# Optimization experiments

Measured on AMD Instinct MI355X. Metric: run time of the kernel, lower is better.

Reference implementation:

```python
import jax, jax.numpy as jnp
import numpy as np
import math

B, S, HID = 2, 1024, 2048
N_HEAD, N_KV = 16, 4
HEAD = HID // N_HEAD          # 128
N_REP = N_HEAD // N_KV        # 4


def setup_inputs() -> dict:
    key = jax.random.key(0)
    ks = jax.random.split(key, 5)
    x = jax.random.normal(ks[0], (B, S, HID), dtype=jnp.float32)
    # realistic RoPE tables: freqs over half dim, duplicated (rotate_half convention)
    inv_freq = 1.0 / (10000.0 ** (np.arange(0, HEAD, 2, dtype=np.float32) / HEAD))
    t = np.arange(S, dtype=np.float32)
    freqs = np.outer(t, inv_freq)                    # [S, HEAD/2]
    emb = np.concatenate([freqs, freqs], axis=-1)    # [S, HEAD]
    cos = jnp.asarray(np.cos(emb), dtype=jnp.float32)
    sin = jnp.asarray(np.sin(emb), dtype=jnp.float32)
    sc = 0.02
    wq = jax.random.normal(ks[1], (HID, HID), dtype=jnp.float32) * sc
    wk = jax.random.normal(ks[2], (HID, N_KV * HEAD), dtype=jnp.float32) * sc
    wv = jax.random.normal(ks[3], (HID, N_KV * HEAD), dtype=jnp.float32) * sc
    wo = jax.random.normal(ks[4], (HID, HID), dtype=jnp.float32) * sc
    return {"x": x, "cos": cos, "sin": sin, "wq": wq, "wk": wk, "wv": wv, "wo": wo}


def _rotate_half(t):
    h = t.shape[-1] // 2
    return jnp.concatenate([-t[..., h:], t[..., :h]], axis=-1)


def reference(x, cos, sin, wq, wk, wv, wo):
    b, s, _ = x.shape
    q = (x @ wq).reshape(b, s, N_HEAD, HEAD)   # [B,S,H,D]
    k = (x @ wk).reshape(b, s, N_KV, HEAD)     # [B,S,Kv,D]
    v = (x @ wv).reshape(b, s, N_KV, HEAD)
    # RoPE: cos/sin [S,D] -> [S,1,D], broadcasts over batch and heads
    c = cos[:s, None, :]
    sn = sin[:s, None, :]
    q = q * c + _rotate_half(q) * sn
    k = k * c + _rotate_half(k) * sn
    # GQA: repeat kv heads to match query heads
    k = jnp.repeat(k, N_REP, axis=2)           # [B,S,H,D]
    v = jnp.repeat(v, N_REP, axis=2)
    q = q.transpose(0, 2, 1, 3)                # [B,H,S,D]
    k = k.transpose(0, 2, 1, 3)
    v = v.transpose(0, 2, 1, 3)
    scores = jnp.einsum("bhqd,bhkd->bhqk", q, k) / math.sqrt(HEAD)
    causal = jnp.triu(jnp.full((s, s), -jnp.inf, dtype=scores.dtype), k=1)
    scores = scores + causal[None, None, :, :]
    probs = jax.nn.softmax(scores.astype(jnp.float32), axis=-1).astype(q.dtype)
    out = jnp.einsum("bhqk,bhkd->bhqd", probs, v)   # [B,H,S,D]
    out = out.transpose(0, 2, 1, 3).reshape(b, s, N_HEAD * HEAD)
    return out @ wo
```

## Files before the change

### kernel.cpp

```cpp
#include <hip/hip_runtime.h>
#include <hip/hip_bf16.h>
#include <math.h>
#include <stdint.h>

#define BATCH 2
#define SEQ   1024
#define HID   2048
#define NH    16
#define NKV   4
#define HEAD  128
#define MROWS (BATCH*SEQ)
#define QSC   0.08838834764831845f

typedef _Float16 f16;
typedef _Float16 f16x8 __attribute__((ext_vector_type(8)));
typedef __fp16   h16x2 __attribute__((ext_vector_type(2)));
typedef float    f32x4 __attribute__((ext_vector_type(4)));

__device__ __forceinline__ void glds16(const void* g, void* l) {
    __builtin_amdgcn_global_load_lds(
        (const __attribute__((address_space(1))) void*)g,
        (__attribute__((address_space(3))) void*)l, 16, 0, 0);
}

__device__ __forceinline__ f32x4 mfma16(f16x8 a, f16x8 b, f32x4 c) {
    return __builtin_amdgcn_mfma_f32_16x16x32_f16(a, b, c, 0, 0, 0);
}

__global__ __launch_bounds__(256)
void prep(const float* __restrict__ x,
          const float* __restrict__ wq, const float* __restrict__ wk,
          const float* __restrict__ wv, const float* __restrict__ wo,
          f16* __restrict__ x16, f16* __restrict__ Wqkvt, f16* __restrict__ Wot)
{
    __shared__ float t[64][65];
    const int bid = blockIdx.x, tid = threadIdx.x;
    if (bid < 4096) {
        int i = bid * 256 + tid;
        float4 v = ((const float4*)x)[i];
        union { ushort4 u; f16 h[4]; } o;
        o.h[0] = (f16)v.x; o.h[1] = (f16)v.y; o.h[2] = (f16)v.z; o.h[3] = (f16)v.w;
        ((ushort4*)x16)[i] = o.u;
        return;
    }
    const float* W; int ld, cs, k0, n0; f16* out;
    if (bid < 5632) {
        int b2 = bid - 4096;
        n0 = (b2 % 48) * 64; k0 = (b2 / 48) * 64; out = Wqkvt;
        if (n0 < 2048)      { W = wq; ld = 2048; cs = n0; }
        else if (n0 < 2560) { W = wk; ld = 512;  cs = n0 - 2048; }
        else                { W = wv; ld = 512;  cs = n0 - 2560; }
    } else {
        int b3 = bid - 5632;
        n0 = (b3 % 32) * 64; k0 = (b3 / 32) * 64; out = Wot;
        W = wo; ld = 2048; cs = n0;
    }
    const int tr = tid >> 4, tc = tid & 15;
    #pragma unroll
    for (int i = 0; i < 4; ++i) {
        int row = tr * 4 + i;
        float4 v = *(const float4*)&W[(size_t)(k0 + row) * ld + cs + tc * 4];
        t[row][tc*4+0] = v.x; t[row][tc*4+1] = v.y;
        t[row][tc*4+2] = v.z; t[row][tc*4+3] = v.w;
    }
    __syncthreads();
    #pragma unroll
    for (int i = 0; i < 4; ++i) {
        int nrow = tr * 4 + i;
        union { ushort4 u; f16 h[4]; } o;
        o.h[0] = (f16)t[tc*4+0][nrow]; o.h[1] = (f16)t[tc*4+1][nrow];
        o.h[2] = (f16)t[tc*4+2][nrow]; o.h[3] = (f16)t[tc*4+3][nrow];
        *(ushort4*)&out[(size_t)(n0 + nrow) * 2048 + k0 + tc * 4] = o.u;
    }
}

template<int MODE>
__global__ __launch_bounds__(256)
void gemm16(const f16* __restrict__ A, const f16* __restrict__ Bt,
            f16* __restrict__ Oq, f16* __restrict__ Ok, f16* __restrict__ Ov,
            float* __restrict__ Of, int ntn)
{
    __shared__ f16 As[2][128 * 64];
    __shared__ f16 Bs[2][64 * 64];
    const int tid   = threadIdx.x;
    const int lane  = tid & 63;
    const int wid   = tid >> 6;
    const int col_l = lane & 15;
    const int hi    = lane >> 4;

    const int nwg = gridDim.x;
    const int cpx = nwg >> 3;
    const int bid = blockIdx.x;
    const int sw  = (bid & 7) * cpx + (bid >> 3);
    const int n0  = (sw % ntn) * 64;
    const int m0  = (sw / ntn) * 128;

    f32x4 acc[2][4];
    #pragma unroll
    for (int mt = 0; mt < 2; ++mt)
        #pragma unroll
        for (int nt = 0; nt < 4; ++nt)
            acc[mt][nt] = (f32x4){0.f, 0.f, 0.f, 0.f};

    auto stage = [&](int buf, int kt) {
        #pragma unroll
        for (int j = 0; j < 4; ++j) {
            int gidx = j * 256 + tid;
            int r = gidx >> 3, g = gidx & 7;
            int gs = (g ^ (r & 7)) << 3;
            glds16(A + (size_t)(m0 + r) * 2048 + kt * 64 + gs,
                   (char*)&As[buf][0] + (size_t)(j * 256 + (wid << 6)) * 16);
        }
        #pragma unroll
        for (int j = 0; j < 2; ++j) {
            int gidx = j * 256 + tid;
            int r = gidx >> 3, g = gidx & 7;
            int gs = (g ^ (r & 7)) << 3;
            glds16(Bt + (size_t)(n0 + r) * 2048 + kt * 64 + gs,
                   (char*)&Bs[buf][0] + (size_t)(j * 256 + (wid << 6)) * 16);
        }
    };

    stage(0, 0);
    stage(1, 1);

    const int ar0 = wid * 32 + col_l;
    const int ar1 = ar0 + 16;

    int cur = 0;
    #pragma unroll 1
    for (int kt = 0; kt < 32; ++kt) {
        if (kt < 31) asm volatile("s_waitcnt vmcnt(6)" ::: "memory");
        else         asm volatile("s_waitcnt vmcnt(0)" ::: "memory");
        __builtin_amdgcn_s_barrier();
        __builtin_amdgcn_sched_barrier(0);

        #pragma unroll
        for (int ks = 0; ks < 2; ++ks) {
            int gr = (ks << 2) | hi;
            f16x8 a0 = *(const f16x8*)&As[cur][ar0 * 64 + ((gr ^ (ar0 & 7)) << 3)];
            f16x8 a1 = *(const f16x8*)&As[cur][ar1 * 64 + ((gr ^ (ar1 & 7)) << 3)];
            #pragma unroll
            for (int nt = 0; nt < 4; ++nt) {
                int br = nt * 16 + col_l;
                f16x8 b = *(const f16x8*)&Bs[cur][br * 64 + ((gr ^ (br & 7)) << 3)];
                acc[0][nt] = mfma16(a0, b, acc[0][nt]);
                acc[1][nt] = mfma16(a1, b, acc[1][nt]);
            }
        }

        asm volatile("s_waitcnt lgkmcnt(0)" ::: "memory");
        __builtin_amdgcn_sched_barrier(0);
        __builtin_amdgcn_s_barrier();
        if (kt + 2 < 32) stage(cur, kt + 2);
        cur ^= 1;
    }

    if (MODE == 0) {
        #pragma unroll
        for (int mt = 0; mt < 2; ++mt)
            #pragma unroll
            for (int r = 0; r < 4; ++r) {
                int grow = m0 + wid * 32 + mt * 16 + hi * 4 + r;
                #pragma unroll
                for (int nt = 0; nt < 4; ++nt)
                    Of[(size_t)grow * 2048 + n0 + nt * 16 + col_l] = acc[mt][nt][r];
            }
    } else if (n0 < 2048) {
        #pragma unroll
        for (int mt = 0; mt < 2; ++mt)
            #pragma unroll
            for (int r = 0; r < 4; ++r) {
                int grow = m0 + wid * 32 + mt * 16 + hi * 4 + r;
                #pragma unroll
                for (int nt = 0; nt < 4; ++nt)
                    Oq[(size_t)grow * 2048 + n0 + nt * 16 + col_l] = (f16)acc[mt][nt][r];
            }
    } else if (n0 < 2560) {
        #pragma unroll
        for (int mt = 0; mt < 2; ++mt)
            #pragma unroll
            for (int r = 0; r < 4; ++r) {
                int grow = m0 + wid * 32 + mt * 16 + hi * 4 + r;
                #pragma unroll
                for (int nt = 0; nt < 4; ++nt)
                    Ok[(size_t)grow * 512 + (n0 - 2048) + nt * 16 + col_l] = (f16)acc[mt][nt][r];
            }
    } else {
        #pragma unroll
        for (int mt = 0; mt < 2; ++mt) {
            int grow0 = m0 + wid * 32 + mt * 16 + hi * 4;
            int bb = grow0 >> 10, s0 = grow0 & (SEQ - 1);
            #pragma unroll
            for (int nt = 0; nt < 4; ++nt) {
                int vcol = (n0 - 2560) + nt * 16 + col_l;
                int kvh = vcol >> 7, d = vcol & 127;
                union { ushort4 u; f16 h[4]; } pv;
                #pragma unroll
                for (int r = 0; r < 4; ++r) pv.h[r] = (f16)acc[mt][nt][r];
                *(ushort4*)&Ov[(size_t)((bb * 4 + kvh) * 128 + d) * 1024 + s0] = pv.u;
            }
        }
    }
}

__global__ __launch_bounds__(256)
void rope_k(f16* __restrict__ k16,
            const float* __restrict__ cosp, const float* __restrict__ sinp)
{
    int t = blockIdx.x * 256 + threadIdx.x;
    int row = t >> 6; int rem = t & 63; int head = rem >> 4; int quad = rem & 15;
    f16* p = k16 + (size_t)row * 512 + head * 128 + quad * 4;
    const int srow = row & (SEQ - 1);
    const int d0 = quad * 4;
    float4 c4 = *(const float4*)&cosp[srow * HEAD + d0];
    float4 s4 = *(const float4*)&sinp[srow * HEAD + d0];
    union { ushort4 u; f16 h[4]; } lo, hv, olo, ohi;
    lo.u = *(ushort4*)p;
    hv.u = *(ushort4*)(p + 64);
    const float c[4] = {c4.x, c4.y, c4.z, c4.w};
    const float s[4] = {s4.x, s4.y, s4.z, s4.w};
    #pragma unroll
    for (int e = 0; e < 4; ++e) {
        float fl = (float)lo.h[e], fh = (float)hv.h[e];
        olo.h[e] = (f16)(fl * c[e] - fh * s[e]);
        ohi.h[e] = (f16)(fh * c[e] + fl * s[e]);
    }
    *(ushort4*)p        = olo.u;
    *(ushort4*)(p + 64) = ohi.u;
}

__global__ __launch_bounds__(256, 2)
void attn16(const f16* __restrict__ q16, const f16* __restrict__ k16,
            const f16* __restrict__ vT,
            const float* __restrict__ cosp, const float* __restrict__ sinp,
            f16* __restrict__ attnb)
{
    __shared__ f16 Ks[2][64 * 128];
    __shared__ f16 Vs[2][128 * 64];

    const int tid   = threadIdx.x;
    const int lane  = tid & 63;
    const int wid   = tid >> 6;
    const int col_l = lane & 15;
    const int hi    = lane >> 4;

    const int bx = blockIdx.x;
    const int r8 = bx >> 8;
    const int c  = bx & 255;
    const int bh = c >> 3;
    const int j8 = c & 7;
    const int qt = r8 ? j8 : (15 - j8);
    const int b  = bh >> 4;
    const int h  = bh & 15;
    const int kv = h >> 2;
    const int qrow = qt * 64 + wid * 16 + col_l;

    f16x8 qf[4];
    {
        const f16* qp = q16 + (size_t)(b * SEQ + qrow) * 2048 + h * 128 + hi * 8;
        f16x8 raw[4];
        #pragma unroll
        for (int ks = 0; ks < 4; ++ks) raw[ks] = *(const f16x8*)&qp[ks * 32];
        #pragma unroll
        for (int ks = 0; ks < 2; ++ks) {
            union { float4 v; float a[4]; } c0, c1, s0, s1;
            const float* cp = cosp + qrow * HEAD + ks * 32 + hi * 8;
            const float* sp = sinp + qrow * HEAD + ks * 32 + hi * 8;
            c0.v = *(const float4*)cp;  c1.v = *(const float4*)(cp + 4);
            s0.v = *(const float4*)sp;  s1.v = *(const float4*)(sp + 4);
            #pragma unroll
            for (int e = 0; e < 8; ++e) {
                float cc = (e < 4) ? c0.a[e & 3] : c1.a[e & 3];
                float sv = (e < 4) ? s0.a[e & 3] : s1.a[e & 3];
                float lo = (float)raw[ks][e], hv = (float)raw[ks + 2][e];
                qf[ks][e]     = (f16)((lo * cc - hv * sv) * QSC);
                qf[ks + 2][e] = (f16)((hv * cc + lo * sv) * QSC);
            }
        }
    }
    const f16* vTg = vT + (size_t)(b * 4 + kv) * 128 * 1024;

    auto stage = [&](int buf, int kt) {
        #pragma unroll
        for (int j = 0; j < 4; ++j) {
            int gidx = j * 256 + tid;
            int r = gidx >> 4, g = gidx & 15;
            glds16(k16 + (size_t)(b * SEQ + kt * 64 + r) * 512 + kv * 128 + ((g ^ (r & 7)) << 3),
                   (char*)&Ks[buf][0] + (size_t)(j * 256 + (wid << 6)) * 16);
        }
        #pragma unroll
        for (int j = 0; j < 4; ++j) {
            int gidx = j * 256 + tid;
            int d = gidx >> 3, g = gidx & 7;
            glds16(vTg + (size_t)d * 1024 + kt * 64 + ((g ^ (d & 7)) << 3),
                   (char*)&Vs[buf][0] + (size_t)(j * 256 + (wid << 6)) * 16);
        }
    };

    f32x4 O[8];
    #pragma unroll
    for (int dt = 0; dt < 8; ++dt) O[dt] = (f32x4){0.f, 0.f, 0.f, 0.f};
    float mrun = -INFINITY, lrun = 0.f;

    const int ntiles = qt + 1;
    stage(0, 0);
    asm volatile("s_waitcnt vmcnt(0)" ::: "memory");
    __syncthreads();

    int cur = 0;
    #pragma unroll 1
    for (int kt = 0; kt < ntiles; ++kt) {
        if (kt + 1 < ntiles) stage(cur ^ 1, kt + 1);

        f32x4 S[4];
        #pragma unroll
        for (int t = 0; t < 4; ++t) S[t] = (f32x4){0.f, 0.f, 0.f, 0.f};
        #pragma unroll
        for (int ks = 0; ks < 4; ++ks) {
            int gr = (ks << 2) | hi;
            #pragma unroll
            for (int t = 0; t < 4; ++t) {
                int rr = t * 16 + col_l;
                f16x8 kf = *(const f16x8*)&Ks[cur][rr * 128 + ((gr ^ (rr & 7)) << 3)];
                S[t] = mfma16(kf, qf[ks], S[t]);
            }
        }
        float p[16];
        #pragma unroll
        for (int t = 0; t < 4; ++t) {
            p[t*4+0] = S[t][0]; p[t*4+1] = S[t][1];
            p[t*4+2] = S[t][2]; p[t*4+3] = S[t][3];
        }

        if (kt == qt) {
            #pragma unroll
            for (int sl = 0; sl < 16; ++sl) {
                int kk = kt * 64 + (sl >> 2) * 16 + hi * 4 + (sl & 3);
                if (kk > qrow) p[sl] = -INFINITY;
            }
        }

        float mt = p[0];
        #pragma unroll
        for (int sl = 1; sl < 16; ++sl) mt = fmaxf(mt, p[sl]);
        mt = fmaxf(mt, __shfl_xor(mt, 16));
        mt = fmaxf(mt, __shfl_xor(mt, 32));
        float mnew = fmaxf(mrun, mt);
        float corr = __expf(mrun - mnew);
        mrun = mnew;
        float ps = 0.f;
        #pragma unroll
        for (int sl = 0; sl < 16; ++sl) { p[sl] = __expf(p[sl] - mnew); ps += p[sl]; }
        ps += __shfl_xor(ps, 16);
        ps += __shfl_xor(ps, 32);
        lrun = lrun * corr + ps;

        union U2 { h16x2 h; int i; };
        int pk[8];
        #pragma unroll
        for (int t = 0; t < 4; ++t) {
            { U2 u; u.h = __builtin_amdgcn_cvt_pkrtz(p[t*4+0], p[t*4+1]); pk[t*2+0] = u.i; }
            { U2 u; u.h = __builtin_amdgcn_cvt_pkrtz(p[t*4+2], p[t*4+3]); pk[t*2+1] = u.i; }
        }
        union UA { f16x8 v; int i[4]; } F0, F1;
        #pragma unroll
        for (int j = 0; j < 4; ++j) {
            int srcl = col_l + 16 * ((2 * hi + (j >> 1)) & 3);
            int a0 = __builtin_amdgcn_ds_bpermute(srcl << 2, pk[j & 1]);
            int a1 = __builtin_amdgcn_ds_bpermute(srcl << 2, pk[2 + (j & 1)]);
            F0.i[j] = (hi >= 2) ? a1 : a0;
            int b0 = __builtin_amdgcn_ds_bpermute(srcl << 2, pk[4 + (j & 1)]);
            int b1 = __builtin_amdgcn_ds_bpermute(srcl << 2, pk[6 + (j & 1)]);
            F1.i[j] = (hi >= 2) ? b1 : b0;
        }

        float cb[4];
        #pragma unroll
        for (int r = 0; r < 4; ++r)
            cb[r] = __int_as_float(__builtin_amdgcn_ds_bpermute((hi * 4 + r) << 2,
                                                                __float_as_int(corr)));
        #pragma unroll
        for (int dt = 0; dt < 8; ++dt) {
            O[dt][0] *= cb[0]; O[dt][1] *= cb[1];
            O[dt][2] *= cb[2]; O[dt][3] *= cb[3];
        }

        #pragma unroll
        for (int dt = 0; dt < 8; ++dt) {
            int vr = dt * 16 + col_l;
            f16x8 v0 = *(const f16x8*)&Vs[cur][vr * 64 + ((hi ^ (vr & 7)) << 3)];
            O[dt] = mfma16(F0.v, v0, O[dt]);
            f16x8 v1 = *(const f16x8*)&Vs[cur][vr * 64 + (((4 | hi) ^ (vr & 7)) << 3)];
            O[dt] = mfma16(F1.v, v1, O[dt]);
        }

        if (kt + 1 < ntiles) {
            asm volatile("s_waitcnt vmcnt(0)" ::: "memory");
            __syncthreads();
            cur ^= 1;
        }
    }

    float linv = 1.f / lrun;
    float lb[4];
    #pragma unroll
    for (int r = 0; r < 4; ++r)
        lb[r] = __int_as_float(__builtin_amdgcn_ds_bpermute((hi * 4 + r) << 2,
                                                            __float_as_int(linv)));
    #pragma unroll
    for (int dt = 0; dt < 8; ++dt)
        #pragma unroll
        for (int r = 0; r < 4; ++r) {
            int row = b * SEQ + qt * 64 + wid * 16 + hi * 4 + r;
            attnb[(size_t)row * 2048 + h * 128 + dt * 16 + col_l] = (f16)(O[dt][r] * lb[r]);
        }
}

extern "C" void kernel_launch(void* const* d_in, const int* in_sizes, int n_in,
                              void* d_out, int out_size, void* d_ws, size_t ws_size,
                              hipStream_t stream)
{
    const float* x    = (const float*)d_in[0];
    const float* cosp = (const float*)d_in[1];
    const float* sinp = (const float*)d_in[2];
    const float* wq   = (const float*)d_in[3];
    const float* wk   = (const float*)d_in[4];
    const float* wv   = (const float*)d_in[5];
    const float* wo   = (const float*)d_in[6];
    float* out = (float*)d_out;

    char* ws = (char*)d_ws;
    f16* x16    = (f16*)(ws);
    f16* attn16v= (f16*)(ws);
    f16* Wqkvt  = (f16*)(ws + 8388608);
    f16* q16    = (f16*)(ws + 20971520);
    f16* k16    = (f16*)(ws + 29360128);
    f16* vT     = (f16*)(ws + 31457280);
    f16* Wot    = (f16*)(ws + 33554432);

    prep<<<6656, 256, 0, stream>>>(x, wq, wk, wv, wo, x16, Wqkvt, Wot);

    gemm16<1><<<768, 256, 0, stream>>>(x16, Wqkvt, q16, k16, vT, nullptr, 48);

    rope_k<<<512, 256, 0, stream>>>(k16, cosp, sinp);

    attn16<<<512, 256, 0, stream>>>(q16, k16, vT, cosp, sinp, attn16v);

    gemm16<0><<<512, 256, 0, stream>>>(attn16v, Wot, nullptr, nullptr, nullptr, out, 32);
}
```

Measured before the change: 203.7 us.

## Give each attention wave two 16-row query groups with lazy softmax rescaling

The attention kernel drops to two waves of 128 threads per block, and each wave now handles 32 query rows as two 16-row groups. Each K and V fragment read from LDS feeds two MFMAs, so LDS traffic per FLOP is roughly halved. It also skips the output rescale when the running max has risen by no more than 8 (a threshold in the lazy style), and raises wave priority around the MFMA sections. The cost is higher register pressure, fewer waves per block for latency hiding, and the staging work falls on fewer threads.

```diff
diff --git a/kernel.cpp b/kernel.cpp
--- a/kernel.cpp
+++ b/kernel.cpp
@@ -230,7 +230,7 @@
     *(ushort4*)(p + 64) = ohi.u;
 }
 
-__global__ __launch_bounds__(256, 2)
+__global__ __launch_bounds__(128)
 void attn16(const f16* __restrict__ q16, const f16* __restrict__ k16,
             const f16* __restrict__ vT,
             const float* __restrict__ cosp, const float* __restrict__ sinp,
@@ -254,10 +254,12 @@
     const int b  = bh >> 4;
     const int h  = bh & 15;
     const int kv = h >> 2;
-    const int qrow = qt * 64 + wid * 16 + col_l;
-
-    f16x8 qf[4];
-    {
+    const int qbase = qt * 64 + wid * 32;
+
+    f16x8 qf[2][4];
+    #pragma unroll
+    for (int g = 0; g < 2; ++g) {
+        const int qrow = qbase + g * 16 + col_l;
         const f16* qp = q16 + (size_t)(b * SEQ + qrow) * 2048 + h * 128 + hi * 8;
         f16x8 raw[4];
         #pragma unroll
@@ -274,8 +276,8 @@
                 float cc = (e < 4) ? c0.a[e & 3] : c1.a[e & 3];
                 float sv = (e < 4) ? s0.a[e & 3] : s1.a[e & 3];
                 float lo = (float)raw[ks][e], hv = (float)raw[ks + 2][e];
-                qf[ks][e]     = (f16)((lo * cc - hv * sv) * QSC);
-                qf[ks + 2][e] = (f16)((hv * cc + lo * sv) * QSC);
+                qf[g][ks][e]     = (f16)((lo * cc - hv * sv) * QSC);
+                qf[g][ks + 2][e] = (f16)((hv * cc + lo * sv) * QSC);
             }
         }
     }
@@ -283,25 +285,27 @@
 
     auto stage = [&](int buf, int kt) {
         #pragma unroll
-        for (int j = 0; j < 4; ++j) {
-            int gidx = j * 256 + tid;
+        for (int j = 0; j < 8; ++j) {
+            int gidx = j * 128 + tid;
             int r = gidx >> 4, g = gidx & 15;
             glds16(k16 + (size_t)(b * SEQ + kt * 64 + r) * 512 + kv * 128 + ((g ^ (r & 7)) << 3),
-                   (char*)&Ks[buf][0] + (size_t)(j * 256 + (wid << 6)) * 16);
-        }
-        #pragma unroll
-        for (int j = 0; j < 4; ++j) {
-            int gidx = j * 256 + tid;
+                   (char*)&Ks[buf][0] + (size_t)(j * 128 + (wid << 6)) * 16);
+        }
+        #pragma unroll
+        for (int j = 0; j < 8; ++j) {
+            int gidx = j * 128 + tid;
             int d = gidx >> 3, g = gidx & 7;
             glds16(vTg + (size_t)d * 1024 + kt * 64 + ((g ^ (d & 7)) << 3),
-                   (char*)&Vs[buf][0] + (size_t)(j * 256 + (wid << 6)) * 16);
+                   (char*)&Vs[buf][0] + (size_t)(j * 128 + (wid << 6)) * 16);
         }
     };
 
-    f32x4 O[8];
-    #pragma unroll
-    for (int dt = 0; dt < 8; ++dt) O[dt] = (f32x4){0.f, 0.f, 0.f, 0.f};
-    float mrun = -INFINITY, lrun = 0.f;
+    f32x4 O[2][8];
+    #pragma unroll
+    for (int g = 0; g < 2; ++g)
+        #pragma unroll
+        for (int dt = 0; dt < 8; ++dt) O[g][dt] = (f32x4){0.f, 0.f, 0.f, 0.f};
+    float m0 = -INFINITY, m1 = -INFINITY, l0 = 0.f, l1 = 0.f;
 
     const int ntiles = qt + 1;
     stage(0, 0);
@@ -313,9 +317,13 @@
     for (int kt = 0; kt < ntiles; ++kt) {
         if (kt + 1 < ntiles) stage(cur ^ 1, kt + 1);
 
-        f32x4 S[4];
-        #pragma unroll
-        for (int t = 0; t < 4; ++t) S[t] = (f32x4){0.f, 0.f, 0.f, 0.f};
+        f32x4 S0[4], S1[4];
+        #pragma unroll
+        for (int t = 0; t < 4; ++t) {
+            S0[t] = (f32x4){0.f, 0.f, 0.f, 0.f};
+            S1[t] = (f32x4){0.f, 0.f, 0.f, 0.f};
+        }
+        __builtin_amdgcn_s_setprio(1);
         #pragma unroll
         for (int ks = 0; ks < 4; ++ks) {
             int gr = (ks << 2) | hi;
@@ -323,77 +331,108 @@
             for (int t = 0; t < 4; ++t) {
                 int rr = t * 16 + col_l;
                 f16x8 kf = *(const f16x8*)&Ks[cur][rr * 128 + ((gr ^ (rr & 7)) << 3)];
-                S[t] = mfma16(kf, qf[ks], S[t]);
-            }
-        }
-        float p[16];
-        #pragma unroll
-        for (int t = 0; t < 4; ++t) {
-            p[t*4+0] = S[t][0]; p[t*4+1] = S[t][1];
-            p[t*4+2] = S[t][2]; p[t*4+3] = S[t][3];
-        }
+                S0[t] = mfma16(kf, qf[0][ks], S0[t]);
+                S1[t] = mfma16(kf, qf[1][ks], S1[t]);
+            }
+        }
+        __builtin_amdgcn_s_setprio(0);
+
+        float p0[16], p1[16];
+        #pragma unroll
+        for (int t = 0; t < 4; ++t)
+            #pragma unroll
+            for (int r = 0; r < 4; ++r) {
+                p0[t*4+r] = S0[t][r];
+                p1[t*4+r] = S1[t][r];
+            }
 
         if (kt == qt) {
             #pragma unroll
             for (int sl = 0; sl < 16; ++sl) {
                 int kk = kt * 64 + (sl >> 2) * 16 + hi * 4 + (sl & 3);
-                if (kk > qrow) p[sl] = -INFINITY;
-            }
-        }
-
-        float mt = p[0];
-        #pragma unroll
-        for (int sl = 1; sl < 16; ++sl) mt = fmaxf(mt, p[sl]);
-        mt = fmaxf(mt, __shfl_xor(mt, 16));
-        mt = fmaxf(mt, __shfl_xor(mt, 32));
-        float mnew = fmaxf(mrun, mt);
-        float corr = __expf(mrun - mnew);
-        mrun = mnew;
-        float ps = 0.f;
-        #pragma unroll
-        for (int sl = 0; sl < 16; ++sl) { p[sl] = __expf(p[sl] - mnew); ps += p[sl]; }
-        ps += __shfl_xor(ps, 16);
-        ps += __shfl_xor(ps, 32);
-        lrun = lrun * corr + ps;
+                if (kk > qbase + col_l)      p0[sl] = -INFINITY;
+                if (kk > qbase + 16 + col_l) p1[sl] = -INFINITY;
+            }
+        }
+
+        float pm0 = p0[0], pm1 = p1[0];
+        #pragma unroll
+        for (int sl = 1; sl < 16; ++sl) { pm0 = fmaxf(pm0, p0[sl]); pm1 = fmaxf(pm1, p1[sl]); }
+        pm0 = fmaxf(pm0, __shfl_xor(pm0, 16)); pm1 = fmaxf(pm1, __shfl_xor(pm1, 16));
+        pm0 = fmaxf(pm0, __shfl_xor(pm0, 32)); pm1 = fmaxf(pm1, __shfl_xor(pm1, 32));
+
+        const bool skip = __all((pm0 <= m0 + 8.f) && (pm1 <= m1 + 8.f));
+        if (!skip) {
+            float mn0 = fmaxf(m0, pm0), mn1 = fmaxf(m1, pm1);
+            float corr0 = __expf(m0 - mn0), corr1 = __expf(m1 - mn1);
+            m0 = mn0; m1 = mn1;
+            float cb0[4], cb1[4];
+            #pragma unroll
+            for (int r = 0; r < 4; ++r) {
+                cb0[r] = __int_as_float(__builtin_amdgcn_ds_bpermute((hi * 4 + r) << 2,
+                                                                     __float_as_int(corr0)));
+                cb1[r] = __int_as_float(__builtin_amdgcn_ds_bpermute((hi * 4 + r) << 2,
+                                                                     __float_as_int(corr1)));
+            }
+            #pragma unroll
+            for (int dt = 0; dt < 8; ++dt)
+                #pragma unroll
+                for (int r = 0; r < 4; ++r) {
+                    O[0][dt][r] *= cb0[r];
+                    O[1][dt][r] *= cb1[r];
+                }
+            l0 *= corr0; l1 *= corr1;
+        }
+
+        float ps0 = 0.f, ps1 = 0.f;
+        #pragma unroll
+        for (int sl = 0; sl < 16; ++sl) {
+            p0[sl] = __expf(p0[sl] - m0); ps0 += p0[sl];
+            p1[sl] = __expf(p1[sl] - m1); ps1 += p1[sl];
+        }
+        ps0 += __shfl_xor(ps0, 16); ps1 += __shfl_xor(ps1, 16);
+        ps0 += __shfl_xor(ps0, 32); ps1 += __shfl_xor(ps1, 32);
+        l0 += ps0; l1 += ps1;
 
         union U2 { h16x2 h; int i; };
-        int pk[8];
+        int pk0[8], pk1[8];
         #pragma unroll
         for (int t = 0; t < 4; ++t) {
-            { U2 u; u.h = __builtin_amdgcn_cvt_pkrtz(p[t*4+0], p[t*4+1]); pk[t*2+0] = u.i; }
-            { U2 u; u.h = __builtin_amdgcn_cvt_pkrtz(p[t*4+2], p[t*4+3]); pk[t*2+1] = u.i; }
-        }
-        union UA { f16x8 v; int i[4]; } F0, F1;
+            { U2 u; u.h = __builtin_amdgcn_cvt_pkrtz(p0[t*4+0], p0[t*4+1]); pk0[t*2+0] = u.i; }
+            { U2 u; u.h = __builtin_amdgcn_cvt_pkrtz(p0[t*4+2], p0[t*4+3]); pk0[t*2+1] = u.i; }
+            { U2 u; u.h = __builtin_amdgcn_cvt_pkrtz(p1[t*4+0], p1[t*4+1]); pk1[t*2+0] = u.i; }
+            { U2 u; u.h = __builtin_amdgcn_cvt_pkrtz(p1[t*4+2], p1[t*4+3]); pk1[t*2+1] = u.i; }
+        }
+        union UA { f16x8 v; int i[4]; } F0a, F0b, F1a, F1b;
         #pragma unroll
         for (int j = 0; j < 4; ++j) {
             int srcl = col_l + 16 * ((2 * hi + (j >> 1)) & 3);
-            int a0 = __builtin_amdgcn_ds_bpermute(srcl << 2, pk[j & 1]);
-            int a1 = __builtin_amdgcn_ds_bpermute(srcl << 2, pk[2 + (j & 1)]);
-            F0.i[j] = (hi >= 2) ? a1 : a0;
-            int b0 = __builtin_amdgcn_ds_bpermute(srcl << 2, pk[4 + (j & 1)]);
-            int b1 = __builtin_amdgcn_ds_bpermute(srcl << 2, pk[6 + (j & 1)]);
-            F1.i[j] = (hi >= 2) ? b1 : b0;
-        }
-
-        float cb[4];
-        #pragma unroll
-        for (int r = 0; r < 4; ++r)
-            cb[r] = __int_as_float(__builtin_amdgcn_ds_bpermute((hi * 4 + r) << 2,
-                                                                __float_as_int(corr)));
-        #pragma unroll
-        for (int dt = 0; dt < 8; ++dt) {
-            O[dt][0] *= cb[0]; O[dt][1] *= cb[1];
-            O[dt][2] *= cb[2]; O[dt][3] *= cb[3];
-        }
-
+            int a0 = __builtin_amdgcn_ds_bpermute(srcl << 2, pk0[j & 1]);
+            int a1 = __builtin_amdgcn_ds_bpermute(srcl << 2, pk0[2 + (j & 1)]);
+            F0a.i[j] = (hi >= 2) ? a1 : a0;
+            int b0 = __builtin_amdgcn_ds_bpermute(srcl << 2, pk0[4 + (j & 1)]);
+            int b1 = __builtin_amdgcn_ds_bpermute(srcl << 2, pk0[6 + (j & 1)]);
+            F0b.i[j] = (hi >= 2) ? b1 : b0;
+            int c0 = __builtin_amdgcn_ds_bpermute(srcl << 2, pk1[j & 1]);
+            int c1 = __builtin_amdgcn_ds_bpermute(srcl << 2, pk1[2 + (j & 1)]);
+            F1a.i[j] = (hi >= 2) ? c1 : c0;
+            int d0 = __builtin_amdgcn_ds_bpermute(srcl << 2, pk1[4 + (j & 1)]);
+            int d1 = __builtin_amdgcn_ds_bpermute(srcl << 2, pk1[6 + (j & 1)]);
+            F1b.i[j] = (hi >= 2) ? d1 : d0;
+        }
+
+        __builtin_amdgcn_s_setprio(1);
         #pragma unroll
         for (int dt = 0; dt < 8; ++dt) {
             int vr = dt * 16 + col_l;
             f16x8 v0 = *(const f16x8*)&Vs[cur][vr * 64 + ((hi ^ (vr & 7)) << 3)];
-            O[dt] = mfma16(F0.v, v0, O[dt]);
             f16x8 v1 = *(const f16x8*)&Vs[cur][vr * 64 + (((4 | hi) ^ (vr & 7)) << 3)];
-            O[dt] = mfma16(F1.v, v1, O[dt]);
-        }
+            O[0][dt] = mfma16(F0a.v, v0, O[0][dt]);
+            O[0][dt] = mfma16(F0b.v, v1, O[0][dt]);
+            O[1][dt] = mfma16(F1a.v, v0, O[1][dt]);
+            O[1][dt] = mfma16(F1b.v, v1, O[1][dt]);
+        }
+        __builtin_amdgcn_s_setprio(0);
 
         if (kt + 1 < ntiles) {
             asm volatile("s_waitcnt vmcnt(0)" ::: "memory");
@@ -402,18 +441,22 @@
         }
     }
 
-    float linv = 1.f / lrun;
-    float lb[4];
-    #pragma unroll
-    for (int r = 0; r < 4; ++r)
-        lb[r] = __int_as_float(__builtin_amdgcn_ds_bpermute((hi * 4 + r) << 2,
-                                                            __float_as_int(linv)));
+    float li0 = 1.f / l0, li1 = 1.f / l1;
+    float lb0[4], lb1[4];
+    #pragma unroll
+    for (int r = 0; r < 4; ++r) {
+        lb0[r] = __int_as_float(__builtin_amdgcn_ds_bpermute((hi * 4 + r) << 2,
+                                                             __float_as_int(li0)));
+        lb1[r] = __int_as_float(__builtin_amdgcn_ds_bpermute((hi * 4 + r) << 2,
+                                                             __float_as_int(li1)));
+    }
     #pragma unroll
     for (int dt = 0; dt < 8; ++dt)
         #pragma unroll
         for (int r = 0; r < 4; ++r) {
-            int row = b * SEQ + qt * 64 + wid * 16 + hi * 4 + r;
-            attnb[(size_t)row * 2048 + h * 128 + dt * 16 + col_l] = (f16)(O[dt][r] * lb[r]);
+            int row0 = b * SEQ + qbase + hi * 4 + r;
+            attnb[(size_t)row0 * 2048 + h * 128 + dt * 16 + col_l]        = (f16)(O[0][dt][r] * lb0[r]);
+            attnb[(size_t)(row0 + 16) * 2048 + h * 128 + dt * 16 + col_l] = (f16)(O[1][dt][r] * lb1[r]);
         }
 }
 
@@ -445,7 +488,7 @@
 
     rope_k<<<512, 256, 0, stream>>>(k16, cosp, sinp);
 
-    attn16<<<512, 256, 0, stream>>>(q16, k16, vT, cosp, sinp, attn16v);
+    attn16<<<512, 128, 0, stream>>>(q16, k16, vT, cosp, sinp, attn16v);
 
     gemm16<0><<<512, 256, 0, stream>>>(attn16v, Wot, nullptr, nullptr, nullptr, out, 32);
 }
```

New measurement: 212.1 us. 1.04x slower.
